# Kernel tuning notes

Measured on AMD Instinct MI355X. Metric: run time of the kernel, lower is better.

The kernel has to match this reference:

```python
import jax, jax.numpy as jnp
import numpy as np

D_MODEL = 1024
EPS_DT = 1e-4
LN_EPS = 1e-5


def _layernorm(y, gamma, beta):
    mu = jnp.mean(y, axis=-1, keepdims=True)
    var = jnp.var(y, axis=-1, keepdims=True)
    return (y - mu) * jax.lax.rsqrt(var + LN_EPS) * gamma + beta


def setup_inputs() -> dict:
    key = jax.random.key(0)
    ks = jax.random.split(key, 8)
    B, T, D = 8, 4096, D_MODEL
    s = 1.0 / np.sqrt(D)  # ~ torch Linear default init scale
    return {
        "x": jax.random.normal(ks[0], (B, T, D), jnp.float32),
        "delta_t": jax.random.uniform(ks[1], (B, T, D), jnp.float32),
        "log_decay": jnp.zeros((D,), jnp.float32),
        "W_in": jax.random.uniform(ks[2], (D, D), jnp.float32, -s, s),
        "b_in": jax.random.uniform(ks[3], (D,), jnp.float32, -s, s),
        "W_gate": jax.random.uniform(ks[4], (D, D), jnp.float32, -s, s),
        "b_gate": jax.random.uniform(ks[5], (D,), jnp.float32, -s, s),
        "W_out": jax.random.uniform(ks[6], (D, D), jnp.float32, -s, s),
        "b_out": jax.random.uniform(ks[7], (D,), jnp.float32, -s, s),
        "gamma": jnp.ones((D,), jnp.float32),
        "beta": jnp.zeros((D,), jnp.float32),
    }


def reference(x, delta_t, log_decay, W_in, b_in, W_gate, b_gate, W_out, b_out, gamma, beta):
    B, T, D = x.shape
    decay = jax.nn.softplus(log_decay) + 1e-4          # [D]
    dt = jnp.maximum(delta_t, EPS_DT)                   # [B,T,D]
    lamb = jnp.exp(-decay * dt)                         # [B,T,D]
    # Drive terms depend only on x -> precompute in parallel (big GEMMs).
    update = jnp.einsum('btd,ed->bte', x, W_in) + b_in
    gate = jax.nn.sigmoid(jnp.einsum('btd,ed->bte', x, W_gate) + b_gate)
    drive = (1.0 - lamb) * gate * update                # [B,T,D]

    def step(state, inputs):
        l_t, d_t = inputs
        state = l_t * state + d_t
        return state, state

    state0 = jnp.zeros((B, D), x.dtype)
    final_state, states = jax.lax.scan(
        step, state0,
        (jnp.swapaxes(lamb, 0, 1), jnp.swapaxes(drive, 0, 1)))
    states = jnp.swapaxes(states, 0, 1)                 # [B,T,D]
    # dropout is identity in eval mode
    y = states + jnp.einsum('btd,ed->bte', states, W_out) + b_out
    out = _layernorm(y, gamma, beta)
    return out, final_state
```

## Files before the change

### kernel.cpp

```cpp
#include <hip/hip_runtime.h>
#include <hip/hip_bf16.h>

#define D_MODEL 1024
#define BATCH 8
#define SEQ 4096
#define MROWS (BATCH*SEQ)
#define NC 64
#define CL 64

typedef __attribute__((ext_vector_type(4))) float f32x4;
typedef __attribute__((ext_vector_type(8))) short s16x8;

__device__ __forceinline__ unsigned short f2bf(float f){
  union { float f; unsigned int u; } v; v.f = f;
  return (unsigned short)((v.u + 0x7fffu + ((v.u >> 16) & 1u)) >> 16);
}
__device__ __forceinline__ float bf2f(unsigned int bits){
  union { unsigned int u; float f; } v; v.u = bits << 16; return v.f;
}

__device__ __forceinline__ void gload16(const void* g, void* l){
  __builtin_amdgcn_global_load_lds(
      (const __attribute__((address_space(1))) unsigned int*)g,
      (__attribute__((address_space(3))) unsigned int*)l, 16, 0, 0);
}

__global__ __launch_bounds__(256)
void prep_all_kernel(const float* __restrict__ x,
                     const float* __restrict__ Wi, const float* __restrict__ Wg,
                     const float* __restrict__ Wo, const float* __restrict__ ld,
                     unsigned short* __restrict__ xb,
                     unsigned short* __restrict__ Wugb,
                     unsigned short* __restrict__ Wob,
                     float* __restrict__ decay, int nx4){
  const int b = blockIdx.x;
  if (b < 8192){
    int i = b*256 + threadIdx.x;
    for (; i < nx4; i += 8192*256){
      float4 v = ((const float4*)x)[i];
      ushort4 o;
      o.x = f2bf(v.x); o.y = f2bf(v.y); o.z = f2bf(v.z); o.w = f2bf(v.w);
      ((ushort4*)xb)[i] = o;
    }
  } else {
    const int i = (b-8192)*256 + threadIdx.x;
    const int row  = i >> 8;
    const int col4 = i & 255;
    const int g    = row >> 6;
    const int r    = row & 63;
    float4 a = ((const float4*)Wi)[i]; ushort4 o;
    o.x=f2bf(a.x); o.y=f2bf(a.y); o.z=f2bf(a.z); o.w=f2bf(a.w);
    ((ushort4*)Wugb)[(g*128 + r)*256 + col4] = o;
    a = ((const float4*)Wg)[i];
    o.x=f2bf(a.x); o.y=f2bf(a.y); o.z=f2bf(a.z); o.w=f2bf(a.w);
    ((ushort4*)Wugb)[(g*128 + 64 + r)*256 + col4] = o;
    a = ((const float4*)Wo)[i];
    o.x=f2bf(a.x); o.y=f2bf(a.y); o.z=f2bf(a.z); o.w=f2bf(a.w); ((ushort4*)Wob)[i]=o;
    if (i < D_MODEL){
      float v = ld[i];
      float sp = fmaxf(v, 0.f) + log1pf(expf(-fabsf(v)));
      decay[i] = sp + 1e-4f;
    }
  }
}

__global__ __launch_bounds__(256, 3)
void gemm_dual64_kernel(const unsigned short* __restrict__ Xb,
                        const unsigned short* __restrict__ Wugb,
                        const float* __restrict__ b_in,
                        const float* __restrict__ b_gate,
                        const float* __restrict__ decay,
                        const float* __restrict__ delta,
                        unsigned int* __restrict__ pack)
{
  __shared__ unsigned short sA[128*64];
  __shared__ unsigned short sB[128*64];
  const int tid  = threadIdx.x;
  const int lane = tid & 63;
  const int wave = tid >> 6;
  const int wr = wave >> 1, wc = wave & 1;
  const int bid  = blockIdx.x;
  const int idx  = bid >> 3;
  const int xcd  = bid & 7;
  const int ct   = idx & 15;
  const int bcol = ct * 64;
  const int brow = (xcd*32 + (idx >> 4)) * 128;

  const f32x4 zero = {0.f,0.f,0.f,0.f};
  f32x4 accU[4][2], accG[4][2];
  #pragma unroll
  for (int a=0;a<4;a++)
    #pragma unroll
    for (int b=0;b<2;b++){ accU[a][b]=zero; accG[a][b]=zero; }

  for (int kt = 0; kt < D_MODEL/64; ++kt){
    __syncthreads();
    #pragma unroll
    for (int i=0;i<4;i++){
      const int ob = i*256 + wave*64;
      const int o  = ob + lane;
      const int r  = o >> 3;
      const int c  = ((o & 7) ^ (r & 7)) * 16;
      gload16((const char*)Xb   + (size_t)(brow + r)*(D_MODEL*2) + (size_t)kt*128 + c,
              (char*)sA + (size_t)ob*16);
      gload16((const char*)Wugb + (size_t)(ct*128 + r)*(D_MODEL*2) + (size_t)kt*128 + c,
              (char*)sB + (size_t)ob*16);
    }
    __syncthreads();
    #pragma unroll
    for (int ks=0; ks<2; ++ks){
      s16x8 af[4], bu[2], bg[2];
      #pragma unroll
      for (int mi=0; mi<4; mi++){
        const int row = wr*64 + mi*16 + (lane & 15);
        const int chunk = (ks*4 + (lane>>4)) ^ (row & 7);
        af[mi] = *(const s16x8*)((const char*)sA + row*128 + chunk*16);
      }
      #pragma unroll
      for (int ni=0; ni<2; ni++){
        const int nu = wc*32 + ni*16 + (lane & 15);
        const int chunk = (ks*4 + (lane>>4)) ^ (nu & 7);
        bu[ni] = *(const s16x8*)((const char*)sB + nu*128 + chunk*16);
        bg[ni] = *(const s16x8*)((const char*)sB + (nu+64)*128 + chunk*16);
      }
      #pragma unroll
      for (int mi=0; mi<4; mi++)
        #pragma unroll
        for (int ni=0; ni<2; ni++){
          accU[mi][ni] = __builtin_amdgcn_mfma_f32_16x16x32_bf16(af[mi], bu[ni], accU[mi][ni], 0,0,0);
          accG[mi][ni] = __builtin_amdgcn_mfma_f32_16x16x32_bf16(af[mi], bg[ni], accG[mi][ni], 0,0,0);
        }
    }
  }

  #pragma unroll
  for (int ni=0; ni<2; ni++){
    const int col = bcol + wc*32 + ni*16 + (lane & 15);
    const float vb = b_in[col], vg = b_gate[col], dc = decay[col];
    #pragma unroll
    for (int mi=0; mi<4; mi++){
      #pragma unroll
      for (int q=0; q<4; q++){
        const int row = brow + wr*64 + mi*16 + ((lane>>4)*4) + q;
        const size_t idx2 = (size_t)row*D_MODEL + col;
        const float u = accU[mi][ni][q] + vb;
        const float z = accG[mi][ni][q] + vg;
        const float g = 1.f/(1.f + __expf(-z));
        const float dt = fmaxf(delta[idx2], 1e-4f);
        const float lam = __expf(-dc*dt);
        const float omla = 1.f - lam;
        const float drv = omla * g * u;
        pack[idx2] = ((unsigned int)f2bf(drv) << 16) | (unsigned int)f2bf(omla);
      }
    }
  }
}

__global__ __launch_bounds__(256)
void scan_passA(const unsigned int* __restrict__ pack, float* __restrict__ cA, float* __restrict__ cB){
  const int d0 = (blockIdx.x*256 + threadIdx.x)*2;
  const int c = blockIdx.y, b = blockIdx.z;
  size_t base = ((size_t)b*SEQ + (size_t)c*CL)*D_MODEL + d0;
  float A0=1.f, A1=1.f, s0=0.f, s1=0.f;
  #pragma unroll 8
  for (int t=0;t<CL;t++){
    uint2 p = *(const uint2*)(pack + base + (size_t)t*D_MODEL);
    float om0 = bf2f(p.x & 0xffffu), dr0 = bf2f(p.x >> 16);
    float om1 = bf2f(p.y & 0xffffu), dr1 = bf2f(p.y >> 16);
    float l0 = 1.f - om0, l1 = 1.f - om1;
    A0 *= l0; A1 *= l1;
    s0 = fmaf(l0, s0, dr0);
    s1 = fmaf(l1, s1, dr1);
  }
  const size_t ci = ((size_t)b*NC + c)*D_MODEL + d0;
  *(float2*)(cA+ci) = make_float2(A0,A1);
  *(float2*)(cB+ci) = make_float2(s0,s1);
}

__global__ __launch_bounds__(256)
void scan_passB(const float* __restrict__ cA, const float* __restrict__ cB,
                float* __restrict__ cS, float* __restrict__ fstate){
  const int d0 = (blockIdx.x*256 + threadIdx.x)*2;
  const int b = blockIdx.y;
  float s0=0.f, s1=0.f;
  for (int c=0;c<NC;c++){
    const size_t ci = ((size_t)b*NC + c)*D_MODEL + d0;
    *(float2*)(cS+ci) = make_float2(s0,s1);
    float2 a  = *(const float2*)(cA+ci);
    float2 bb = *(const float2*)(cB+ci);
    s0 = fmaf(a.x, s0, bb.x);
    s1 = fmaf(a.y, s1, bb.y);
  }
  *(float2*)(fstate + (size_t)b*D_MODEL + d0) = make_float2(s0,s1);
}

__global__ __launch_bounds__(256)
void scan_passC(const unsigned int* __restrict__ pack, const float* __restrict__ cS,
                unsigned short* __restrict__ statesb){
  const int d0 = (blockIdx.x*256 + threadIdx.x)*2;
  const int c = blockIdx.y, b = blockIdx.z;
  float2 sv = *(const float2*)(cS + ((size_t)b*NC + c)*D_MODEL + d0);
  float s0 = sv.x, s1 = sv.y;
  size_t base = ((size_t)b*SEQ + (size_t)c*CL)*D_MODEL + d0;
  #pragma unroll 8
  for (int t=0;t<CL;t++){
    uint2 p = *(const uint2*)(pack + base + (size_t)t*D_MODEL);
    float om0 = bf2f(p.x & 0xffffu), dr0 = bf2f(p.x >> 16);
    float om1 = bf2f(p.y & 0xffffu), dr1 = bf2f(p.y >> 16);
    s0 = fmaf(-om0, s0, s0) + dr0;
    s1 = fmaf(-om1, s1, s1) + dr1;
    unsigned int w = ((unsigned int)f2bf(s1) << 16) | (unsigned int)f2bf(s0);
    *(unsigned int*)(statesb + base + (size_t)t*D_MODEL) = w;
  }
}

__global__ __launch_bounds__(256, 3)
void gemm_out_kernel(const unsigned short* __restrict__ Sb,
                     const unsigned short* __restrict__ Wob,
                     const float* __restrict__ b_out,
                     unsigned short* __restrict__ yb)
{
  __shared__ unsigned short sA[128*64];
  __shared__ unsigned short sB[128*64];
  const int tid  = threadIdx.x;
  const int lane = tid & 63;
  const int wave = tid >> 6;
  const int wr = wave >> 1, wc = wave & 1;
  const int bid = blockIdx.x;
  const int swz = ((bid & 7) << 8) | (bid >> 3);
  const int bcol = (swz & 7) * 128;
  const int brow = (swz >> 3) * 128;

  const f32x4 zero = {0.f,0.f,0.f,0.f};
  f32x4 acc[4][4];
  #pragma unroll
  for (int a=0;a<4;a++)
    #pragma unroll
    for (int b=0;b<4;b++) acc[a][b]=zero;

  const int kt_res = (bcol >> 6) + wc;

  for (int kt = 0; kt < D_MODEL/64; ++kt){
    __syncthreads();
    #pragma unroll
    for (int i=0;i<4;i++){
      const int ob = i*256 + wave*64;
      const int o  = ob + lane;
      const int r  = o >> 3;
      const int c  = ((o & 7) ^ (r & 7)) * 16;
      gload16((const char*)Sb  + (size_t)(brow + r)*(D_MODEL*2) + (size_t)kt*128 + c,
              (char*)sA + (size_t)ob*16);
      gload16((const char*)Wob + (size_t)(bcol + r)*(D_MODEL*2) + (size_t)kt*128 + c,
              (char*)sB + (size_t)ob*16);
    }
    __syncthreads();
    #pragma unroll
    for (int ks=0; ks<2; ++ks){
      s16x8 af[4], bf[4];
      #pragma unroll
      for (int mi=0; mi<4; mi++){
        const int row = wr*64 + mi*16 + (lane & 15);
        const int chunk = (ks*4 + (lane>>4)) ^ (row & 7);
        af[mi] = *(const s16x8*)((const char*)sA + row*128 + chunk*16);
      }
      #pragma unroll
      for (int ni=0; ni<4; ni++){
        const int n = wc*64 + ni*16 + (lane & 15);
        const int chunk = (ks*4 + (lane>>4)) ^ (n & 7);
        bf[ni] = *(const s16x8*)((const char*)sB + n*128 + chunk*16);
      }
      #pragma unroll
      for (int mi=0; mi<4; mi++)
        #pragma unroll
        for (int ni=0; ni<4; ni++)
          acc[mi][ni] = __builtin_amdgcn_mfma_f32_16x16x32_bf16(af[mi], bf[ni], acc[mi][ni], 0,0,0);
    }
    if (kt == kt_res){
      #pragma unroll
      for (int ni=0; ni<4; ni++){
        #pragma unroll
        for (int mi=0; mi<4; mi++){
          #pragma unroll
          for (int q=0; q<4; q++){
            const int rl = wr*64 + mi*16 + ((lane>>4)*4) + q;
            const int cl = ni*16 + (lane & 15);
            const int byte = rl*128 + (((cl>>3) ^ (rl&7))*16) + ((cl&7)*2);
            acc[mi][ni][q] += bf2f((unsigned int)*(const unsigned short*)((const char*)sA + byte));
          }
        }
      }
    }
  }

  #pragma unroll
  for (int ni=0; ni<4; ni++){
    const int col = bcol + wc*64 + ni*16 + (lane & 15);
    const float vb = b_out[col];
    #pragma unroll
    for (int mi=0; mi<4; mi++){
      #pragma unroll
      for (int q=0; q<4; q++){
        const int row = brow + wr*64 + mi*16 + ((lane>>4)*4) + q;
        yb[(size_t)row*D_MODEL + col] = f2bf(acc[mi][ni][q] + vb);
      }
    }
  }
}

__global__ __launch_bounds__(256)
void ln_kernel(const unsigned short* __restrict__ yb,
               const float* __restrict__ gamma, const float* __restrict__ beta,
               float* __restrict__ out)
{
  const int row = blockIdx.x;
  const int tid = threadIdx.x;
  ushort4 yv = ((const ushort4*)(yb + (size_t)row*D_MODEL))[tid];
  float4 v;
  v.x = bf2f(yv.x); v.y = bf2f(yv.y); v.z = bf2f(yv.z); v.w = bf2f(yv.w);
  float s = v.x+v.y+v.z+v.w;
  float q = v.x*v.x + v.y*v.y + v.z*v.z + v.w*v.w;
  #pragma unroll
  for (int off=32; off>0; off>>=1){ s += __shfl_xor(s, off); q += __shfl_xor(q, off); }
  __shared__ float rs[4], rq[4];
  const int wave = tid>>6, lane = tid&63;
  if (lane==0){ rs[wave]=s; rq[wave]=q; }
  __syncthreads();
  float ts = rs[0]+rs[1]+rs[2]+rs[3];
  float tq = rq[0]+rq[1]+rq[2]+rq[3];
  float mu  = ts * (1.f/D_MODEL);
  float var = tq * (1.f/D_MODEL) - mu*mu;
  float inv = rsqrtf(var + 1e-5f);
  float4 g = ((const float4*)gamma)[tid];
  float4 b = ((const float4*)beta)[tid];
  float4 o;
  o.x = (v.x-mu)*inv*g.x + b.x;
  o.y = (v.y-mu)*inv*g.y + b.y;
  o.z = (v.z-mu)*inv*g.z + b.z;
  o.w = (v.w-mu)*inv*g.w + b.w;
  ((float4*)(out + (size_t)row*D_MODEL))[tid] = o;
}

extern "C" void kernel_launch(void* const* d_in, const int* in_sizes, int n_in,
                              void* d_out, int out_size, void* d_ws, size_t ws_size,
                              hipStream_t stream) {
  const float* x         = (const float*)d_in[0];
  const float* delta     = (const float*)d_in[1];
  const float* log_decay = (const float*)d_in[2];
  const float* W_in      = (const float*)d_in[3];
  const float* b_in      = (const float*)d_in[4];
  const float* W_gate    = (const float*)d_in[5];
  const float* b_gate    = (const float*)d_in[6];
  const float* W_out     = (const float*)d_in[7];
  const float* b_out     = (const float*)d_in[8];
  const float* gamma     = (const float*)d_in[9];
  const float* beta      = (const float*)d_in[10];

  char* w = (char*)d_ws;
  unsigned short* xb   = (unsigned short*)(w);
  unsigned short* Wugb = (unsigned short*)(w + 67108864);
  unsigned short* Wob  = (unsigned short*)(w + 71303168);
  float*          decay= (float*)        (w + 73400320);
  float*          cA   = (float*)        (w + 73404416);
  float*          cB   = (float*)        (w + 75501568);
  float*          cS   = (float*)        (w + 77598720);
  unsigned int*   pack = (unsigned int*) (w + 79695872);
  unsigned short* ybuf = (unsigned short*)pack;
  unsigned short* statesb = xb;

  float* out    = (float*)d_out;
  float* fstate = out + (size_t)MROWS*D_MODEL;

  hipLaunchKernelGGL(prep_all_kernel, dim3(9216), dim3(256), 0, stream,
                     x, W_in, W_gate, W_out, log_decay, xb, Wugb, Wob, decay, MROWS*D_MODEL/4);
  hipLaunchKernelGGL(gemm_dual64_kernel, dim3(4096), dim3(256), 0, stream,
                     xb, Wugb, b_in, b_gate, decay, delta, pack);
  hipLaunchKernelGGL(scan_passA, dim3(2,NC,BATCH), dim3(256), 0, stream, pack, cA, cB);
  hipLaunchKernelGGL(scan_passB, dim3(2,BATCH), dim3(256), 0, stream, cA, cB, cS, fstate);
  hipLaunchKernelGGL(scan_passC, dim3(2,NC,BATCH), dim3(256), 0, stream, pack, cS, statesb);
  hipLaunchKernelGGL(gemm_out_kernel, dim3(2048), dim3(256), 0, stream,
                     statesb, Wob, b_out, ybuf);
  hipLaunchKernelGGL(ln_kernel, dim3(MROWS), dim3(256), 0, stream, ybuf, gamma, beta, out);
}
```

Baseline: 404.3 us.

## Fuse chunk-level scan reduction into dual GEMM epilogue, drop scan_passA

The dual GEMM epilogue now computes each 64-row chunk's (A, B) scan summary in registers, using per-lane serial combines plus cross-lane shuffles, and writes cA/cB directly. This removes the separate scan_passA kernel, which re-read the whole packed bf16 buffer (128 MB) from memory. It uses bf16-rounded values so the summaries match what passC reads, at the cost of extra ALU and shuffle work in the GEMM epilogue.

```diff
diff --git a/kernel.cpp b/kernel.cpp
--- a/kernel.cpp
+++ b/kernel.cpp
@@ -71,7 +71,8 @@
                         const float* __restrict__ b_gate,
                         const float* __restrict__ decay,
                         const float* __restrict__ delta,
-                        unsigned int* __restrict__ pack)
+                        unsigned int* __restrict__ pack,
+                        float* __restrict__ cA, float* __restrict__ cB)
 {
   __shared__ unsigned short sA[128*64];
   __shared__ unsigned short sB[128*64];
@@ -133,48 +134,57 @@
     }
   }
 
+  const int t0 = brow + wr*64;
+  const int bb = t0 >> 12;
+  const int cc = (t0 & 4095) >> 6;
+  const int g  = lane >> 4;
+
   #pragma unroll
   for (int ni=0; ni<2; ni++){
     const int col = bcol + wc*32 + ni*16 + (lane & 15);
     const float vb = b_in[col], vg = b_gate[col], dc = decay[col];
+    float runA = 1.f, runB = 0.f;
     #pragma unroll
     for (int mi=0; mi<4; mi++){
+      float segA = 1.f, segB = 0.f;
       #pragma unroll
       for (int q=0; q<4; q++){
-        const int row = brow + wr*64 + mi*16 + ((lane>>4)*4) + q;
+        const int row = brow + wr*64 + mi*16 + g*4 + q;
         const size_t idx2 = (size_t)row*D_MODEL + col;
         const float u = accU[mi][ni][q] + vb;
         const float z = accG[mi][ni][q] + vg;
-        const float g = 1.f/(1.f + __expf(-z));
+        const float gt = 1.f/(1.f + __expf(-z));
         const float dt = fmaxf(delta[idx2], 1e-4f);
         const float lam = __expf(-dc*dt);
         const float omla = 1.f - lam;
-        const float drv = omla * g * u;
-        pack[idx2] = ((unsigned int)f2bf(drv) << 16) | (unsigned int)f2bf(omla);
-      }
-    }
-  }
-}
-
-__global__ __launch_bounds__(256)
-void scan_passA(const unsigned int* __restrict__ pack, float* __restrict__ cA, float* __restrict__ cB){
-  const int d0 = (blockIdx.x*256 + threadIdx.x)*2;
-  const int c = blockIdx.y, b = blockIdx.z;
-  size_t base = ((size_t)b*SEQ + (size_t)c*CL)*D_MODEL + d0;
-  float A0=1.f, A1=1.f, s0=0.f, s1=0.f;
-  #pragma unroll 8
-  for (int t=0;t<CL;t++){
-    uint2 p = *(const uint2*)(pack + base + (size_t)t*D_MODEL);
-    float om0 = bf2f(p.x & 0xffffu), dr0 = bf2f(p.x >> 16);
-    float om1 = bf2f(p.y & 0xffffu), dr1 = bf2f(p.y >> 16);
-    float l0 = 1.f - om0, l1 = 1.f - om1;
-    A0 *= l0; A1 *= l1;
-    s0 = fmaf(l0, s0, dr0);
-    s1 = fmaf(l1, s1, dr1);
-  }
-  const size_t ci = ((size_t)b*NC + c)*D_MODEL + d0;
-  *(float2*)(cA+ci) = make_float2(A0,A1);
-  *(float2*)(cB+ci) = make_float2(s0,s1);
+        const float drv = omla * gt * u;
+        const unsigned short omb = f2bf(omla);
+        const unsigned short drb = f2bf(drv);
+        pack[idx2] = ((unsigned int)drb << 16) | (unsigned int)omb;
+        const float lam_q = 1.f - bf2f((unsigned int)omb);
+        const float dr_q  = bf2f((unsigned int)drb);
+        segA *= lam_q;
+        segB = fmaf(lam_q, segB, dr_q);
+      }
+      {
+        float pA = __shfl_xor(segA, 16);
+        float pB = __shfl_xor(segB, 16);
+        if (g & 1){ segB = fmaf(pB, segA, segB); segA = pA * segA; }
+        else      { segB = fmaf(segB, pA, pB);   segA = segA * pA; }
+        pA = __shfl_xor(segA, 32);
+        pB = __shfl_xor(segB, 32);
+        if (g & 2){ segB = fmaf(pB, segA, segB); segA = pA * segA; }
+        else      { segB = fmaf(segB, pA, pB);   segA = segA * pA; }
+      }
+      runB = fmaf(runB, segA, segB);
+      runA *= segA;
+    }
+    if (g == 0){
+      const size_t ci = ((size_t)bb*NC + cc)*D_MODEL + col;
+      cA[ci] = runA;
+      cB[ci] = runB;
+    }
+  }
 }
 
 __global__ __launch_bounds__(256)
@@ -373,8 +383,7 @@
   hipLaunchKernelGGL(prep_all_kernel, dim3(9216), dim3(256), 0, stream,
                      x, W_in, W_gate, W_out, log_decay, xb, Wugb, Wob, decay, MROWS*D_MODEL/4);
   hipLaunchKernelGGL(gemm_dual64_kernel, dim3(4096), dim3(256), 0, stream,
-                     xb, Wugb, b_in, b_gate, decay, delta, pack);
-  hipLaunchKernelGGL(scan_passA, dim3(2,NC,BATCH), dim3(256), 0, stream, pack, cA, cB);
+                     xb, Wugb, b_in, b_gate, decay, delta, pack, cA, cB);
   hipLaunchKernelGGL(scan_passB, dim3(2,BATCH), dim3(256), 0, stream, cA, cB, cS, fstate);
   hipLaunchKernelGGL(scan_passC, dim3(2,NC,BATCH), dim3(256), 0, stream, pack, cS, statesb);
   hipLaunchKernelGGL(gemm_out_kernel, dim3(2048), dim3(256), 0, stream,
```

After: 399.5 us, median of 2. No clear change (-1.2%).
